# Kernel optimization log

Measured on AMD Instinct MI355X. Metric: run time of the kernel, lower is better.

Reference implementation:

```python
import jax, jax.numpy as jnp
import numpy as np

B, N = 2, 6
FC, FH, FW = 256, 32, 88            # encoder feature shape
ORFH, ORFW = 256, 704               # original image H, W
OUT_C = 128
D_ST, D_END, D_STEP = 1.0, 60.0, 3.0
NXV, NYV, NZV = 256, 256, 1         # BEV voxel grid (x, y, z)
DXV = np.array([0.4, 0.4, 20.0], np.float32)          # dx
BXV = np.array([-51.0, -51.0, 0.0], np.float32)       # bx = bound_lo + dx/2
BN_EPS = 1e-3


def _conv(x, w, b):
    y = jax.lax.conv_general_dilated(x, w, (1, 1), 'SAME',
                                     dimension_numbers=('NCHW', 'OIHW', 'NCHW'))
    return y + b[None, :, None, None]


def _bn(x, scale, bias, mean, var):
    inv = scale / jnp.sqrt(var + BN_EPS)
    return x * inv[None, :, None, None] + (bias - mean * inv)[None, :, None, None]


def _frustum():
    ds = jnp.arange(D_ST, D_END, D_STEP, dtype=jnp.float32)      # (D,)
    xs = jnp.linspace(0.0, ORFW - 1.0, FW)
    ys = jnp.linspace(0.0, ORFH - 1.0, FH)
    f = jnp.stack(jnp.broadcast_arrays(xs[None, None, :], ys[None, :, None],
                                       ds[:, None, None]), axis=-1)  # (D,FH,FW,3)
    return f, ds


def _forward(cam2ego_rot, cam2ego_trans, cam_intrins, post_cam2ego_rot,
             post_cam2ego_trans, img_feats,
             conv1_w, conv1_b, bn1_s, bn1_b, bn1_m, bn1_v,
             conv2_w, conv2_b, bn2_s, bn2_b, bn2_m, bn2_v,
             conv3_w, conv3_b):
    frustum, depth_vals = _frustum()
    D = depth_vals.shape[0]
    # ---- geometry (GaussianLSS.get_geometry) ----
    pts = frustum[None, None] - post_cam2ego_trans[:, :, None, None, None, :]
    inv_post = jnp.linalg.inv(post_cam2ego_rot)                       # (B,N,3,3)
    pts = jnp.einsum('bnij,bndhwj->bndhwi', inv_post, pts)
    pts = jnp.concatenate([pts[..., :2] * pts[..., 2:3], pts[..., 2:3]], -1)
    combine = cam2ego_rot @ jnp.linalg.inv(cam_intrins)
    geometry = (jnp.einsum('bnij,bndhwj->bndhwi', combine, pts)
                + cam2ego_trans[:, :, None, None, None, :])           # (B,N,D,H,W,3)
    # ---- depth net + gaussian depth distribution (get_cam_feature) ----
    x = img_feats.reshape(B * N, FC, FH, FW)
    x = jax.nn.relu(_bn(_conv(x, conv1_w, conv1_b), bn1_s, bn1_b, bn1_m, bn1_v))
    x = jax.nn.relu(_bn(_conv(x, conv2_w, conv2_b), bn2_s, bn2_b, bn2_m, bn2_v))
    x = _conv(x, conv3_w, conv3_b)                                    # (BN, OUT_C+2, H, W)
    mu, log_sigma, feats = x[:, 0], x[:, 1], x[:, 2:]
    sigma = jnp.exp(log_sigma) + 1e-6
    g = jnp.exp(-0.5 * (depth_vals[None, :, None, None] - mu[:, None]) ** 2
                / (sigma[:, None] ** 2))                              # (BN,D,H,W)
    g = g / (jnp.sum(g, axis=1, keepdims=True) + 1e-6)
    vol = g[:, None] * feats[:, :, None]                              # (BN,C,D,H,W)
    vol = vol.reshape(B, N, OUT_C, D, FH, FW).transpose(0, 1, 3, 4, 5, 2)  # (B,N,D,H,W,C)
    # ---- bev_pool: voxelize + scatter-add ----
    dx = jnp.asarray(DXV)
    bx = jnp.asarray(BXV)
    geom = ((geometry - (bx - dx / 2.0)) / dx).astype(jnp.int32)      # trunc like .long()
    gx, gy, gz = geom[..., 0], geom[..., 1], geom[..., 2]
    kept = ((gx >= 0) & (gx < NXV) & (gy >= 0) & (gy < NYV)
            & (gz >= 0) & (gz < NZV))                                 # (B,N,D,H,W)
    bidx = jnp.arange(B, dtype=jnp.int32)[:, None, None, None, None]
    flat = ((bidx * NZV + gz) * NXV + gx) * NYV + gy
    flat = jnp.where(kept, flat, 0)
    w = kept.astype(vol.dtype)
    data = (vol * w[..., None]).reshape(-1, OUT_C)
    bev = jax.ops.segment_sum(data, flat.reshape(-1),
                              num_segments=B * NZV * NXV * NYV)
    # torch: (B,C,Z,X,Y) -> cat(unbind(dim=2), 1) -> (B, Z*C, X, Y)
    bev = bev.reshape(B, NZV, NXV, NYV, OUT_C).transpose(0, 1, 4, 2, 3)
    bev = bev.reshape(B, NZV * OUT_C, NXV, NYV)
    # ---- ref_bev_pool mask ----
    counts = jax.ops.segment_sum(w.reshape(-1), flat.reshape(-1),
                                 num_segments=B * NZV * NXV * NYV)
    mask = jnp.any(counts.reshape(B, NZV, NXV, NYV) > 0, axis=1)      # (B,X,Y) bool
    return bev, mask


def setup_inputs() -> dict:
    key = jax.random.key(0)
    ks = jax.random.split(key, 16)
    # camera->ego rotation: cam z -> ego x, cam x -> -ego y, cam y -> -ego z
    R = jnp.array([[0., 0., 1.], [-1., 0., 0.], [0., -1., 0.]], jnp.float32)
    cam2ego_rot = jnp.tile(R, (B, N, 1, 1)) + 0.01 * jax.random.normal(ks[0], (B, N, 3, 3))
    cam2ego_trans = jax.random.uniform(ks[1], (B, N, 3), minval=-2.0, maxval=2.0)
    K = jnp.array([[500., 0., ORFW / 2.], [0., 500., ORFH / 2.], [0., 0., 1.]], jnp.float32)
    cam_intrins = jnp.tile(K, (B, N, 1, 1))
    post_cam2ego_rot = jnp.tile(jnp.eye(3, dtype=jnp.float32), (B, N, 1, 1)) \
        + 0.005 * jax.random.normal(ks[2], (B, N, 3, 3))
    post_cam2ego_trans = 0.5 * jax.random.normal(ks[3], (B, N, 3))
    img_feats = 0.1 * jax.random.normal(ks[4], (B, N, FC, FH, FW))
    conv3_b = jnp.zeros((OUT_C + 2,)).at[0].set(25.0).at[1].set(2.3)  # mu~25m, sigma~10m
    return dict(
        cam2ego_rot=cam2ego_rot, cam2ego_trans=cam2ego_trans,
        cam_intrins=cam_intrins, post_cam2ego_rot=post_cam2ego_rot,
        post_cam2ego_trans=post_cam2ego_trans, img_feats=img_feats,
        conv1_w=0.02 * jax.random.normal(ks[5], (FC, FC, 3, 3)),
        conv1_b=jnp.zeros((FC,)),
        bn1_s=1.0 + 0.01 * jax.random.normal(ks[6], (FC,)),
        bn1_b=0.01 * jax.random.normal(ks[7], (FC,)),
        bn1_m=0.01 * jax.random.normal(ks[8], (FC,)),
        bn1_v=1.0 + 0.1 * jax.random.uniform(ks[9], (FC,)),
        conv2_w=0.02 * jax.random.normal(ks[10], (FC, FC, 3, 3)),
        conv2_b=jnp.zeros((FC,)),
        bn2_s=1.0 + 0.01 * jax.random.normal(ks[11], (FC,)),
        bn2_b=0.01 * jax.random.normal(ks[12], (FC,)),
        bn2_m=0.01 * jax.random.normal(ks[13], (FC,)),
        bn2_v=1.0 + 0.1 * jax.random.uniform(ks[14], (FC,)),
        conv3_w=0.02 * jax.random.normal(ks[15], (OUT_C + 2, FC, 1, 1)),
        conv3_b=conv3_b,
    )


def reference(cam2ego_rot, cam2ego_trans, cam_intrins, post_cam2ego_rot,
              post_cam2ego_trans, img_feats,
              conv1_w, conv1_b, bn1_s, bn1_b, bn1_m, bn1_v,
              conv2_w, conv2_b, bn2_s, bn2_b, bn2_m, bn2_v,
              conv3_w, conv3_b):
    return _forward(cam2ego_rot, cam2ego_trans, cam_intrins, post_cam2ego_rot,
                    post_cam2ego_trans, img_feats,
                    conv1_w, conv1_b, bn1_s, bn1_b, bn1_m, bn1_v,
                    conv2_w, conv2_b, bn2_s, bn2_b, bn2_m, bn2_v,
                    conv3_w, conv3_b)
```

## Files before the change

### kernel.cpp

```cpp
#include <hip/hip_runtime.h>
#include <math.h>

typedef unsigned short ushort_t;
typedef unsigned int uint_t;

#define NIMG 12
#define NCH  256
#define FH   32
#define FW   88
#define NPIX 2816
#define NDEP 20
#define NOUTC 128
#define NVOX 65536
#define NPTS 675840
#define NKEY 131072
#define BEV_FLOATS 16777216u

#define B_OCC    0u
#define B_A1     4096u
#define B_C1     5120u
#define B_A2     6144u
#define B_C2     7168u
#define B_TOT    278528u
#define B_FEAT   282624u
#define B_RECS   17584128u
#define B_BEV    22990848u
#define B_VCODE  22990848u
#define B_WT     25694208u
#define B_CNT    28397568u
#define B_OFFS   28921856u
#define B_CUR    29446144u
#define B_SPINE  29970432u
#define B_XBF    29972480u
#define B_ACT1   47273984u
#define B_ACT2   64575488u
#define B_WSWZ1  81876992u
#define B_WSWZ2  83056640u
#define B_WSWZ3  84236288u

#define PREP_W2    2304
#define PREP_W3    4608
#define PREP_BN    4752
#define PREP_CAST0 4753
#define PREP_GEOM0 5281
#define PREP_NBLK  7921

typedef __attribute__((ext_vector_type(8))) short bf16x8;
typedef __attribute__((ext_vector_type(4))) float floatx4;
typedef __attribute__((ext_vector_type(4))) uint_t u32x4;

__device__ __forceinline__ ushort_t f2bf(float f) {
    uint_t x = __float_as_uint(f);
    return (ushort_t)((x + 0x7fffu + ((x >> 16) & 1u)) >> 16);
}
__device__ __forceinline__ float bf2f(ushort_t u) {
    return __uint_as_float(((uint_t)u) << 16);
}

__device__ __forceinline__ void inv3x3(const float* __restrict__ M, float* __restrict__ o) {
    float a=M[0],b=M[1],c=M[2],d=M[3],e=M[4],f=M[5],g=M[6],h=M[7],i=M[8];
    float A = e*i - f*h;
    float B = c*h - b*i;
    float C = b*f - c*e;
    float D = f*g - d*i;
    float E = a*i - c*g;
    float F = c*d - a*f;
    float G = d*h - e*g;
    float H = b*g - a*h;
    float I = a*e - b*d;
    float det = a*A + b*D + c*G;
    float id = 1.0f / det;
    o[0]=A*id; o[1]=B*id; o[2]=C*id;
    o[3]=D*id; o[4]=E*id; o[5]=F*id;
    o[6]=G*id; o[7]=H*id; o[8]=I*id;
}

__device__ __forceinline__ void wprep_one(
    const float* __restrict__ w, ushort_t* __restrict__ dst,
    int ntap, int ncib, int ncog, int nco, int nci, int idx, bool split)
{
    int j = idx & 7;
    int l = (idx >> 3) & 63;
    int pairidx = idx >> 9;
    int g = pairidx % ncog;
    int b = (pairidx / ncog) % ncib;
    int t = pairidx / (ncog * ncib);
    int co = g * 16 + (l & 15);
    int ci = b * 32 + (l >> 4) * 8 + j;
    float v = 0.0f;
    if (co < nco) v = w[((size_t)co * nci + ci) * ntap + t];
    ushort_t hi = f2bf(v);
    if (split) {
        dst[(size_t)pairidx * 1024 + l * 8 + j]       = hi;
        dst[(size_t)pairidx * 1024 + 512 + l * 8 + j] = f2bf(v - bf2f(hi));
    } else {
        dst[(size_t)pairidx * 512 + l * 8 + j] = hi;
    }
}

__global__ __launch_bounds__(256) void prep_all_kernel(
    const float* __restrict__ w1, ushort_t* __restrict__ d1,
    const float* __restrict__ w2, ushort_t* __restrict__ d2,
    const float* __restrict__ w3, ushort_t* __restrict__ d3,
    const float* __restrict__ c2e_rot, const float* __restrict__ c2e_trans,
    const float* __restrict__ intrins, const float* __restrict__ post_rot,
    const float* __restrict__ post_trans,
    const float* __restrict__ c1b, const float* __restrict__ s1,
    const float* __restrict__ bb1, const float* __restrict__ m1, const float* __restrict__ v1,
    const float* __restrict__ c2b, const float* __restrict__ s2,
    const float* __restrict__ bb2, const float* __restrict__ m2, const float* __restrict__ v2,
    float* __restrict__ A1, float* __restrict__ C1,
    float* __restrict__ A2, float* __restrict__ C2,
    const float* __restrict__ img_in, ushort_t* __restrict__ xbf_out,
    int* __restrict__ vcode, uint_t* __restrict__ cnt)
{
    __shared__ __align__(16) ushort_t clds[64 * 264];
    int bid = blockIdx.x;
    int t = threadIdx.x;
    if (bid < PREP_W2) {
        wprep_one(w1, d1, 9, 8, 16, 256, 256, bid * 256 + t, false);
    } else if (bid < PREP_W3) {
        wprep_one(w2, d2, 9, 8, 16, 256, 256, (bid - PREP_W2) * 256 + t, false);
    } else if (bid < PREP_BN) {
        int idx = (bid - PREP_W3) * 256 + t;
        if (idx < 36864) wprep_one(w3, d3, 1, 8, 9, 130, 256, idx, true);
    } else if (bid == PREP_BN) {
        float i1 = s1[t] / sqrtf(v1[t] + 1e-3f);
        A1[t] = i1;
        C1[t] = (c1b[t] - m1[t]) * i1 + bb1[t];
        float i2 = s2[t] / sqrtf(v2[t] + 1e-3f);
        A2[t] = i2;
        C2[t] = (c2b[t] - m2[t]) * i2 + bb2[t];
    } else if (bid < PREP_GEOM0) {
        int cblk = bid - PREP_CAST0;
        int img = cblk / 44;
        int px0 = (cblk - img * 44) * 64;
        const float* src = img_in + (size_t)img * NCH * NPIX;
        int pxl = t & 63;
        int cib = t >> 6;
        #pragma unroll 4
        for (int cc = 0; cc < 64; ++cc) {
            int ci = cc * 4 + cib;
            float v = src[(size_t)ci * NPIX + px0 + pxl];
            clds[pxl * 264 + ci] = f2bf(v);
        }
        __syncthreads();
        int wv = t >> 6, lane = t & 63;
        uint2* outv = (uint2*)xbf_out;
        #pragma unroll
        for (int i = 0; i < 16; ++i) {
            int p = wv * 16 + i;
            uint2 val = *(const uint2*)&clds[p * 264 + lane * 4];
            outv[(size_t)(img * NPIX + px0 + p) * 64 + lane] = val;
        }
    } else {
        int i = (bid - PREP_GEOM0) * 256 + t;
        int lane = t & 63;
        int hw  = i % NPIX;
        int tmp = i / NPIX;
        int d   = tmp % NDEP;
        int bn  = tmp / NDEP;
        int h = hw / FW, w = hw - h * FW;
        float ip[9], ki[9], comb[9];
        inv3x3(post_rot + bn * 9, ip);
        inv3x3(intrins  + bn * 9, ki);
        const float* R = c2e_rot + bn * 9;
        #pragma unroll
        for (int r = 0; r < 3; ++r)
            #pragma unroll
            for (int cc = 0; cc < 3; ++cc)
                comb[r*3+cc] = R[r*3+0]*ki[0*3+cc] + R[r*3+1]*ki[1*3+cc] + R[r*3+2]*ki[2*3+cc];
        float xs = (float)w * (703.0f / 87.0f);
        float ys = (float)h * (255.0f / 31.0f);
        float dv = 1.0f + 3.0f * (float)d;
        float fx = xs - post_trans[bn*3+0];
        float fy = ys - post_trans[bn*3+1];
        float fz = dv - post_trans[bn*3+2];
        float p0 = ip[0]*fx + ip[1]*fy + ip[2]*fz;
        float p1 = ip[3]*fx + ip[4]*fy + ip[5]*fz;
        float p2 = ip[6]*fx + ip[7]*fy + ip[8]*fz;
        p0 *= p2; p1 *= p2;
        float gx = comb[0]*p0 + comb[1]*p1 + comb[2]*p2 + c2e_trans[bn*3+0];
        float gy = comb[3]*p0 + comb[4]*p1 + comb[5]*p2 + c2e_trans[bn*3+1];
        float gz = comb[6]*p0 + comb[7]*p1 + comb[8]*p2 + c2e_trans[bn*3+2];
        const float cx = -51.0f - 0.2f, cy = -51.0f - 0.2f, cz = 0.0f - 10.0f;
        int ix = (int)((gx - cx) / 0.4f);
        int iy = (int)((gy - cy) / 0.4f);
        int iz = (int)((gz - cz) / 20.0f);
        bool kept = (ix >= 0) && (ix < 256) && (iy >= 0) && (iy < 256) && (iz == 0);
        int code = kept ? ((ix << 8) | iy) : -1;
        vcode[i] = code;

        int b = bn / 6;
        uint_t key = kept ? (uint_t)((b << 16) | code) : 0xFFFFFFFFu;
        uint_t prevkey = __shfl_up(key, 1);
        bool leader = (lane == 0) || (key != prevkey);
        unsigned long long mask = __ballot(leader);
        if (leader && kept) {
            unsigned long long higher = mask & ~((2ULL << lane) - 1ULL);
            int nxt = higher ? (__ffsll((long long)higher) - 1) : 64;
            atomicAdd(&cnt[key], (uint_t)(nxt - lane));
        }
    }
}

__global__ __launch_bounds__(256, 3) void conv3x3_mfma(
    const ushort_t* __restrict__ in,
    const ushort_t* __restrict__ wswz,
    const float* __restrict__ Abn, const float* __restrict__ Cbn,
    ushort_t* __restrict__ out)
{
    __shared__ __align__(16) ushort_t lds[2][8640];
    int bx = blockIdx.x;
    int cg = blockIdx.y;
    int img = bx >> 5, h = bx & 31;
    int t = threadIdx.x;
    int w = t >> 6, l = t & 63;
    int q = l >> 4, c = l & 15;
    const int n0s[6] = {0, 16, 32, 48, 64, 72};

    for (int i = t; i < 8640; i += 256) ((uint_t*)lds)[i] = 0;

    const u32x4* src4 = (const u32x4*)(in + (size_t)img * NPIX * 256);
    const bf16x8* wsA = (const bf16x8*)wswz;

    int gbase[5], loff[5];
    bool sval[5];
    #pragma unroll
    for (int k = 0; k < 5; ++k) {
        int p = t + k * 256;
        bool valid = (p < 1056);
        int chunk = p >> 2, sub = p & 3;
        int r = chunk / 88;
        int col = chunk - r * 88;
        int hin = h - 1 + r;
        bool inb = valid && (hin >= 0) && (hin < FH);
        sval[k] = inb;
        gbase[k] = inb ? ((hin * 88 + col) * 32 + sub) : 0;
        int cs = col + 1;
        int slot = sub ^ ((cs >> 1) & 3);
        loff[k] = ((r * 90 + cs) * 4 + slot) * 8;
    }

    floatx4 acc[2][6];
    #pragma unroll
    for (int m = 0; m < 2; ++m)
        #pragma unroll
        for (int n = 0; n < 6; ++n)
            acc[m][n] = (floatx4){0.f, 0.f, 0.f, 0.f};

    int g0 = cg * 8 + w * 2;

    __syncthreads();
    #pragma unroll
    for (int k = 0; k < 5; ++k)
        if (sval[k]) *(u32x4*)&lds[0][loff[k]] = src4[gbase[k]];

    int buf = 0;
    for (int kb = 0; kb < 8; ++kb) {
        __syncthreads();
        u32x4 sreg[5];
        if (kb < 7) {
            #pragma unroll
            for (int k = 0; k < 5; ++k)
                if (sval[k]) sreg[k] = src4[gbase[k] + (kb + 1) * 4];
        }
        const bf16x8* B = (const bf16x8*)lds[buf];

        bf16x8 a0, a1;
        {
            int pa = (0 * 8 + kb) * 16;
            a0 = wsA[(size_t)(pa + g0    ) * 64 + l];
            a1 = wsA[(size_t)(pa + g0 + 1) * 64 + l];
        }
        #pragma unroll
        for (int t9 = 0; t9 < 9; ++t9) {
            bf16x8 na0, na1;
            if (t9 < 8) {
                int pa = ((t9 + 1) * 8 + kb) * 16;
                na0 = wsA[(size_t)(pa + g0    ) * 64 + l];
                na1 = wsA[(size_t)(pa + g0 + 1) * 64 + l];
            }
            int ky = t9 / 3, kx = t9 - ky * 3;
            #pragma unroll
            for (int n = 0; n < 6; ++n) {
                int col = n0s[n] + kx + c;
                int slot = q ^ ((col >> 1) & 3);
                bf16x8 b = B[(ky * 90 + col) * 4 + slot];
                acc[0][n] = __builtin_amdgcn_mfma_f32_16x16x32_bf16(a0, b, acc[0][n], 0, 0, 0);
                acc[1][n] = __builtin_amdgcn_mfma_f32_16x16x32_bf16(a1, b, acc[1][n], 0, 0, 0);
            }
            if (t9 < 8) { a0 = na0; a1 = na1; }
        }
        if (kb < 7) {
            #pragma unroll
            for (int k = 0; k < 5; ++k)
                if (sval[k]) *(u32x4*)&lds[buf ^ 1][loff[k]] = sreg[k];
        }
        buf ^= 1;
    }

    #pragma unroll
    for (int m = 0; m < 2; ++m) {
        int cob = cg * 128 + w * 32 + m * 16 + q * 4;
        float ba0 = Abn[cob+0], ba1 = Abn[cob+1], ba2 = Abn[cob+2], ba3 = Abn[cob+3];
        float bc0 = Cbn[cob+0], bc1 = Cbn[cob+1], bc2 = Cbn[cob+2], bc3 = Cbn[cob+3];
        #pragma unroll
        for (int n = 0; n < 6; ++n) {
            if (n == 5 && c < 8) continue;
            int col = n0s[n] + c;
            floatx4 v = acc[m][n];
            uint_t lo = (uint_t)f2bf(fmaxf(v[0]*ba0+bc0, 0.f)) | ((uint_t)f2bf(fmaxf(v[1]*ba1+bc1, 0.f)) << 16);
            uint_t hi = (uint_t)f2bf(fmaxf(v[2]*ba2+bc2, 0.f)) | ((uint_t)f2bf(fmaxf(v[3]*ba3+bc3, 0.f)) << 16);
            uint2 val; val.x = lo; val.y = hi;
            *(uint2*)&out[((size_t)img * NPIX + h * 88 + col) * 256 + cob] = val;
        }
    }
}

__global__ __launch_bounds__(256, 4) void gemm1x1_mfma(
    const ushort_t* __restrict__ act2,
    const ushort_t* __restrict__ wswz3,
    const float* __restrict__ b3,
    ushort_t* __restrict__ feat, float* __restrict__ wt)
{
    int t = threadIdx.x, wv = t >> 6, l = t & 63, q = l >> 4, c = l & 15;
    int n0 = (blockIdx.x * 4 + wv) * 16;
    int px = n0 + c;
    const bf16x8* A = (const bf16x8*)wswz3;
    const bf16x8* B = (const bf16x8*)act2;
    floatx4 acc[9];
    #pragma unroll
    for (int g = 0; g < 9; ++g) acc[g] = (floatx4){0.f, 0.f, 0.f, 0.f};
    for (int kb = 0; kb < 8; ++kb) {
        bf16x8 b = B[(size_t)px * 32 + kb * 4 + q];
        #pragma unroll
        for (int g = 0; g < 9; ++g) {
            size_t pa = (size_t)(kb * 9 + g) * 128;
            acc[g] = __builtin_amdgcn_mfma_f32_16x16x32_bf16(A[pa + l],      b, acc[g], 0, 0, 0);
            acc[g] = __builtin_amdgcn_mfma_f32_16x16x32_bf16(A[pa + 64 + l], b, acc[g], 0, 0, 0);
        }
    }
    #pragma unroll
    for (int g = 0; g < 9; ++g) {
        #pragma unroll
        for (int r = 0; r < 4; ++r) {
            int co = g * 16 + q * 4 + r;
            if (co < 2 || co >= 130) continue;
            feat[(size_t)px * 128 + (co - 2)] = f2bf(acc[g][r] + b3[co]);
        }
    }
    float muv = acc[0][0] + b3[0];
    float lsv = acc[0][1] + b3[1];
    float mu_b  = __shfl(muv, c);
    float sig   = expf(__shfl(lsv, c)) + 1e-6f;
    float ninv2 = -0.5f / (sig * sig);
    float g5[5]; float s = 0.0f;
    #pragma unroll
    for (int j = 0; j < 5; ++j) {
        float dv = 1.0f + 3.0f * (float)(q * 5 + j);
        float df = dv - mu_b;
        g5[j] = expf(df * df * ninv2);
        s += g5[j];
    }
    s += __shfl_xor(s, 16);
    s += __shfl_xor(s, 32);
    float inv = 1.0f / (s + 1e-6f);
    #pragma unroll
    for (int j = 0; j < 5; ++j)
        wt[(size_t)px * NDEP + q * 5 + j] = g5[j] * inv;
}

__global__ __launch_bounds__(256) void scan_block_kernel(
    const uint_t* __restrict__ cnt, uint_t* __restrict__ offs, uint_t* __restrict__ spine)
{
    __shared__ uint_t s[256];
    int t = threadIdx.x;
    int i = blockIdx.x * 256 + t;
    uint_t v = cnt[i];
    s[t] = v;
    __syncthreads();
    #pragma unroll
    for (int off = 1; off < 256; off <<= 1) {
        uint_t add = (t >= off) ? s[t - off] : 0u;
        __syncthreads();
        s[t] += add;
        __syncthreads();
    }
    offs[i] = s[t] - v;
    if (t == 255) spine[blockIdx.x] = s[255];
}

__global__ __launch_bounds__(256) void fixup_kernel(
    uint_t* __restrict__ offs, const uint_t* __restrict__ spine,
    uint_t* __restrict__ cursor, const uint_t* __restrict__ cnt,
    float* __restrict__ mask_out, uint_t* __restrict__ total,
    unsigned char* __restrict__ occ)
{
    __shared__ uint_t red[256];
    int bid = blockIdx.x, t = threadIdx.x;
    uint_t part = 0;
    for (int j = t; j < bid; j += 256) part += spine[j];
    red[t] = part;
    __syncthreads();
    #pragma unroll
    for (int off = 128; off > 0; off >>= 1) {
        if (t < off) red[t] += red[t + off];
        __syncthreads();
    }
    uint_t prefix = red[0];
    int i = bid * 256 + t;
    uint_t o = offs[i] + prefix;
    offs[i] = o;
    cursor[i] = o;
    uint_t n = cnt[i];
    mask_out[i] = (n > 0) ? 1.0f : 0.0f;
    int lane = t & 63, wv = t >> 6;
    unsigned long long any = __ballot(n > 0u);
    if (lane == 0) occ[bid * 4 + wv] = any ? 1 : 0;
    if (i == NKEY - 1) *total = o + n;
}

__global__ __launch_bounds__(256) void scatter_kernel(
    const int* __restrict__ vcode, const float* __restrict__ wt,
    uint_t* __restrict__ cursor, uint2* __restrict__ recs)
{
    int i = blockIdx.x * 256 + threadIdx.x;
    int lane = threadIdx.x & 63;
    int code = vcode[i];
    int hw  = i % NPIX;
    int tmp = i / NPIX;
    int d   = tmp % NDEP;
    int bn  = tmp / NDEP;
    int b   = bn / 6;
    int gp  = bn * NPIX + hw;
    bool active = (code >= 0);
    uint_t key = active ? (uint_t)((b << 16) | code) : 0xFFFFFFFFu;
    uint2 r;
    r.x = ((uint_t)(code & 0xffff) << 16) | (uint_t)gp;
    r.y = active ? __float_as_uint(wt[(size_t)gp * NDEP + d]) : 0u;

    uint_t prevkey = __shfl_up(key, 1);
    bool leader = (lane == 0) || (key != prevkey);
    unsigned long long mask = __ballot(leader);
    uint_t base = 0;
    if (leader && active) {
        unsigned long long higher = mask & ~((2ULL << lane) - 1ULL);
        int nxt = higher ? (__ffsll((long long)higher) - 1) : 64;
        base = atomicAdd(&cursor[key], (uint_t)(nxt - lane));
    }
    unsigned long long lower = mask & ((2ULL << lane) - 1ULL);
    int lead = 63 - __clzll((long long)lower);
    base = __shfl(base, lead);
    if (active) recs[base + (lane - lead)] = r;
}

__global__ __launch_bounds__(256) void segreduce_kernel(
    const uint2* __restrict__ recs, const uint_t* __restrict__ total,
    const uint_t* __restrict__ featu,
    float* __restrict__ bev_tmp)
{
    uint_t R = *total;
    int wid = blockIdx.x * 4 + (threadIdx.x >> 6);
    uint_t start = (uint_t)wid * 64u;
    if (start >= R) return;
    int lane = threadIdx.x & 63;
    uint_t ustart = __builtin_amdgcn_readfirstlane(start);

    uint_t myidx = ustart + (uint_t)lane;
    if (myidx >= R) myidx = R - 1u;
    uint2 mr = recs[myidx];

    uint_t rx0 = (uint_t)__shfl((int)mr.x, 0);
    uint_t gp00 = rx0 & 0xffffu;
    uint_t prevk = ((gp00 >= 16896u) ? 0x10000u : 0u) | (rx0 >> 16);
    float acc0 = 0.f, acc1 = 0.f;

    uint_t fbuf[2][16];
    #pragma unroll
    for (int j = 0; j < 16; ++j) {
        uint_t rx = (uint_t)__shfl((int)mr.x, j);
        fbuf[0][j] = featu[(size_t)(rx & 0xffffu) * 64 + lane];
    }
    #pragma unroll
    for (int b = 0; b < 4; ++b) {
        if (b < 3) {
            #pragma unroll
            for (int j = 0; j < 16; ++j) {
                uint_t rx = (uint_t)__shfl((int)mr.x, (b + 1) * 16 + j);
                fbuf[(b + 1) & 1][j] = featu[(size_t)(rx & 0xffffu) * 64 + lane];
            }
        }
        #pragma unroll
        for (int j = 0; j < 16; ++j) {
            int e = b * 16 + j;
            uint_t rx = (uint_t)__shfl((int)mr.x, e);
            uint_t ry = (uint_t)__shfl((int)mr.y, e);
            uint_t gp = rx & 0xffffu;
            uint_t key = ((gp >= 16896u) ? 0x10000u : 0u) | (rx >> 16);
            float wv = __uint_as_float(ry);
            if (ustart + (uint_t)e >= R) { key = prevk; wv = 0.f; }
            if (key != prevk) {
                float* p = bev_tmp + (size_t)prevk * NOUTC;
                atomicAdd(p + 2 * lane,     acc0);
                atomicAdd(p + 2 * lane + 1, acc1);
                acc0 = acc1 = 0.f;
                prevk = key;
            }
            uint_t fv = fbuf[b & 1][j];
            acc0 = fmaf(wv, bf2f((ushort_t)(fv & 0xffffu)), acc0);
            acc1 = fmaf(wv, bf2f((ushort_t)(fv >> 16)),     acc1);
        }
    }
    float* p = bev_tmp + (size_t)prevk * NOUTC;
    atomicAdd(p + 2 * lane,     acc0);
    atomicAdd(p + 2 * lane + 1, acc1);
}

__global__ __launch_bounds__(256) void transpose_kernel(
    const float* __restrict__ bev_tmp, const unsigned char* __restrict__ occ,
    float* __restrict__ bev_out)
{
    __shared__ float lds[64 * 129];
    int blk = blockIdx.x;
    int b   = blk >> 10;
    int v0  = (blk & 1023) * 64;
    int t   = threadIdx.x;
    float* dst = bev_out + (size_t)b * NOUTC * NVOX + v0;
    if (!occ[blk]) {
        #pragma unroll
        for (int k = 0; k < 32; ++k) {
            int idx = k * 256 + t;
            int vl = idx & 63, ch = idx >> 6;
            dst[(size_t)ch * NVOX + vl] = 0.0f;
        }
        return;
    }
    const float* src = bev_tmp + ((size_t)b * NVOX + v0) * NOUTC;
    #pragma unroll
    for (int k = 0; k < 32; ++k) {
        int idx = k * 256 + t;
        int v = idx >> 7, ch = idx & 127;
        lds[v * 129 + ch] = src[idx];
    }
    __syncthreads();
    #pragma unroll
    for (int k = 0; k < 32; ++k) {
        int idx = k * 256 + t;
        int vl = idx & 63, ch = idx >> 6;
        dst[(size_t)ch * NVOX + vl] = lds[vl * 129 + ch];
    }
}

extern "C" void kernel_launch(void* const* d_in, const int* in_sizes, int n_in,
                              void* d_out, int out_size, void* d_ws, size_t ws_size,
                              hipStream_t stream) {
    const float* c2e_rot    = (const float*)d_in[0];
    const float* c2e_trans  = (const float*)d_in[1];
    const float* intrins    = (const float*)d_in[2];
    const float* post_rot   = (const float*)d_in[3];
    const float* post_trans = (const float*)d_in[4];
    const float* img_feats  = (const float*)d_in[5];
    const float* conv1_w    = (const float*)d_in[6];
    const float* conv1_b    = (const float*)d_in[7];
    const float* bn1_s = (const float*)d_in[8];
    const float* bn1_b = (const float*)d_in[9];
    const float* bn1_m = (const float*)d_in[10];
    const float* bn1_v = (const float*)d_in[11];
    const float* conv2_w = (const float*)d_in[12];
    const float* conv2_b = (const float*)d_in[13];
    const float* bn2_s = (const float*)d_in[14];
    const float* bn2_b = (const float*)d_in[15];
    const float* bn2_m = (const float*)d_in[16];
    const float* bn2_v = (const float*)d_in[17];
    const float* conv3_w = (const float*)d_in[18];
    const float* conv3_b = (const float*)d_in[19];

    char* base = (char*)d_ws;
    unsigned char* occ = (unsigned char*)(base + B_OCC);
    float*    A1     = (float*)(base + B_A1);
    float*    C1     = (float*)(base + B_C1);
    float*    A2     = (float*)(base + B_A2);
    float*    C2     = (float*)(base + B_C2);
    uint_t*   total  = (uint_t*)(base + B_TOT);
    ushort_t* feat   = (ushort_t*)(base + B_FEAT);
    uint2*    recs   = (uint2*)(base + B_RECS);
    float*    bevtmp = (float*)(base + B_BEV);
    int*      vcode  = (int*)(base + B_VCODE);
    float*    wt     = (float*)(base + B_WT);
    uint_t*   cnt    = (uint_t*)(base + B_CNT);
    uint_t*   offs   = (uint_t*)(base + B_OFFS);
    uint_t*   cursor = (uint_t*)(base + B_CUR);
    uint_t*   spine  = (uint_t*)(base + B_SPINE);
    ushort_t* xbf    = (ushort_t*)(base + B_XBF);
    ushort_t* act1   = (ushort_t*)(base + B_ACT1);
    ushort_t* act2   = (ushort_t*)(base + B_ACT2);
    ushort_t* wswz1  = (ushort_t*)(base + B_WSWZ1);
    ushort_t* wswz2  = (ushort_t*)(base + B_WSWZ2);
    ushort_t* wswz3  = (ushort_t*)(base + B_WSWZ3);

    float* bev_out  = (float*)d_out;
    float* mask_out = bev_out + BEV_FLOATS;

    hipMemsetAsync(cnt, 0, NKEY * sizeof(uint_t), stream);
    prep_all_kernel<<<PREP_NBLK, 256, 0, stream>>>(
        conv1_w, wswz1, conv2_w, wswz2, conv3_w, wswz3,
        c2e_rot, c2e_trans, intrins, post_rot, post_trans,
        conv1_b, bn1_s, bn1_b, bn1_m, bn1_v,
        conv2_b, bn2_s, bn2_b, bn2_m, bn2_v,
        A1, C1, A2, C2,
        img_feats, xbf, vcode, cnt);
    conv3x3_mfma<<<dim3(NIMG * 32, 2), 256, 0, stream>>>(xbf,  wswz1, A1, C1, act1);
    conv3x3_mfma<<<dim3(NIMG * 32, 2), 256, 0, stream>>>(act1, wswz2, A2, C2, act2);
    gemm1x1_mfma<<<528, 256, 0, stream>>>(act2, wswz3, conv3_b, feat, wt);
    scan_block_kernel<<<NKEY / 256, 256, 0, stream>>>(cnt, offs, spine);
    fixup_kernel<<<NKEY / 256, 256, 0, stream>>>(offs, spine, cursor, cnt, mask_out, total, occ);
    scatter_kernel<<<NPTS / 256, 256, 0, stream>>>(vcode, wt, cursor, recs);
    hipMemsetAsync(bevtmp, 0, (size_t)BEV_FLOATS * sizeof(float), stream);
    segreduce_kernel<<<(NPTS / 64 + 3) / 4, 256, 0, stream>>>(recs, total, (const uint_t*)feat, bevtmp);
    transpose_kernel<<<2048, 256, 0, stream>>>(bevtmp, occ, bev_out);
}
```

Measured before the change: 351.0 us.

## Accumulate BEV directly in output layout; fuse block scan into 1x1 GEMM launch

The segmented reduction now atomically adds into the channel-major output, which removes the temporary voxel-major BEV buffer, its memset, the occupancy flags and the transpose kernel. The per-block scan of voxel counts runs as extra blocks of the 1x1 GEMM launch, saving one kernel launch. The depth-weight array is stored depth-major so the scatter reads it in a coalesced way. In exchange, the atomics are now strided by NVOX per channel, so each wave's 64 lanes hit scattered addresses instead of one contiguous row.

Result: slower. 506.4 us (+44.3%).

```diff
diff --git a/kernel.cpp b/kernel.cpp
--- a/kernel.cpp
+++ b/kernel.cpp
@@ -14,9 +14,9 @@
 #define NVOX 65536
 #define NPTS 675840
 #define NKEY 131072
+#define NGP  33792
 #define BEV_FLOATS 16777216u
 
-#define B_OCC    0u
 #define B_A1     4096u
 #define B_C1     5120u
 #define B_A2     6144u
@@ -24,7 +24,6 @@
 #define B_TOT    278528u
 #define B_FEAT   282624u
 #define B_RECS   17584128u
-#define B_BEV    22990848u
 #define B_VCODE  22990848u
 #define B_WT     25694208u
 #define B_CNT    28397568u
@@ -44,6 +43,9 @@
 #define PREP_CAST0 4753
 #define PREP_GEOM0 5281
 #define PREP_NBLK  7921
+
+#define GS_SCAN0   528
+#define GS_NBLK    1040
 
 typedef __attribute__((ext_vector_type(8))) short bf16x8;
 typedef __attribute__((ext_vector_type(4))) float floatx4;
@@ -318,13 +320,34 @@
     }
 }
 
-__global__ __launch_bounds__(256, 4) void gemm1x1_mfma(
+__global__ __launch_bounds__(256, 4) void gemm_scan_kernel(
     const ushort_t* __restrict__ act2,
     const ushort_t* __restrict__ wswz3,
     const float* __restrict__ b3,
-    ushort_t* __restrict__ feat, float* __restrict__ wt)
-{
-    int t = threadIdx.x, wv = t >> 6, l = t & 63, q = l >> 4, c = l & 15;
+    ushort_t* __restrict__ feat, float* __restrict__ wt,
+    const uint_t* __restrict__ cnt, uint_t* __restrict__ offs,
+    uint_t* __restrict__ spine)
+{
+    __shared__ uint_t s[256];
+    int t = threadIdx.x;
+    if (blockIdx.x >= GS_SCAN0) {
+        int blk = blockIdx.x - GS_SCAN0;
+        int i = blk * 256 + t;
+        uint_t v = cnt[i];
+        s[t] = v;
+        __syncthreads();
+        #pragma unroll
+        for (int off = 1; off < 256; off <<= 1) {
+            uint_t add = (t >= off) ? s[t - off] : 0u;
+            __syncthreads();
+            s[t] += add;
+            __syncthreads();
+        }
+        offs[i] = s[t] - v;
+        if (t == 255) spine[blk] = s[255];
+        return;
+    }
+    int wv = t >> 6, l = t & 63, q = l >> 4, c = l & 15;
     int n0 = (blockIdx.x * 4 + wv) * 16;
     int px = n0 + c;
     const bf16x8* A = (const bf16x8*)wswz3;
@@ -355,47 +378,26 @@
     float mu_b  = __shfl(muv, c);
     float sig   = expf(__shfl(lsv, c)) + 1e-6f;
     float ninv2 = -0.5f / (sig * sig);
-    float g5[5]; float s = 0.0f;
+    float g5[5]; float sum = 0.0f;
     #pragma unroll
     for (int j = 0; j < 5; ++j) {
         float dv = 1.0f + 3.0f * (float)(q * 5 + j);
         float df = dv - mu_b;
         g5[j] = expf(df * df * ninv2);
-        s += g5[j];
-    }
-    s += __shfl_xor(s, 16);
-    s += __shfl_xor(s, 32);
-    float inv = 1.0f / (s + 1e-6f);
+        sum += g5[j];
+    }
+    sum += __shfl_xor(sum, 16);
+    sum += __shfl_xor(sum, 32);
+    float inv = 1.0f / (sum + 1e-6f);
     #pragma unroll
     for (int j = 0; j < 5; ++j)
-        wt[(size_t)px * NDEP + q * 5 + j] = g5[j] * inv;
-}
-
-__global__ __launch_bounds__(256) void scan_block_kernel(
-    const uint_t* __restrict__ cnt, uint_t* __restrict__ offs, uint_t* __restrict__ spine)
-{
-    __shared__ uint_t s[256];
-    int t = threadIdx.x;
-    int i = blockIdx.x * 256 + t;
-    uint_t v = cnt[i];
-    s[t] = v;
-    __syncthreads();
-    #pragma unroll
-    for (int off = 1; off < 256; off <<= 1) {
-        uint_t add = (t >= off) ? s[t - off] : 0u;
-        __syncthreads();
-        s[t] += add;
-        __syncthreads();
-    }
-    offs[i] = s[t] - v;
-    if (t == 255) spine[blockIdx.x] = s[255];
+        wt[(size_t)(q * 5 + j) * NGP + px] = g5[j] * inv;
 }
 
 __global__ __launch_bounds__(256) void fixup_kernel(
     uint_t* __restrict__ offs, const uint_t* __restrict__ spine,
     uint_t* __restrict__ cursor, const uint_t* __restrict__ cnt,
-    float* __restrict__ mask_out, uint_t* __restrict__ total,
-    unsigned char* __restrict__ occ)
+    float* __restrict__ mask_out, uint_t* __restrict__ total)
 {
     __shared__ uint_t red[256];
     int bid = blockIdx.x, t = threadIdx.x;
@@ -415,9 +417,6 @@
     cursor[i] = o;
     uint_t n = cnt[i];
     mask_out[i] = (n > 0) ? 1.0f : 0.0f;
-    int lane = t & 63, wv = t >> 6;
-    unsigned long long any = __ballot(n > 0u);
-    if (lane == 0) occ[bid * 4 + wv] = any ? 1 : 0;
     if (i == NKEY - 1) *total = o + n;
 }
 
@@ -438,7 +437,7 @@
     uint_t key = active ? (uint_t)((b << 16) | code) : 0xFFFFFFFFu;
     uint2 r;
     r.x = ((uint_t)(code & 0xffff) << 16) | (uint_t)gp;
-    r.y = active ? __float_as_uint(wt[(size_t)gp * NDEP + d]) : 0u;
+    r.y = active ? __float_as_uint(wt[(size_t)d * NGP + gp]) : 0u;
 
     uint_t prevkey = __shfl_up(key, 1);
     bool leader = (lane == 0) || (key != prevkey);
@@ -458,7 +457,7 @@
 __global__ __launch_bounds__(256) void segreduce_kernel(
     const uint2* __restrict__ recs, const uint_t* __restrict__ total,
     const uint_t* __restrict__ featu,
-    float* __restrict__ bev_tmp)
+    float* __restrict__ bev_out)
 {
     uint_t R = *total;
     int wid = blockIdx.x * 4 + (threadIdx.x >> 6);
@@ -501,9 +500,10 @@
             float wv = __uint_as_float(ry);
             if (ustart + (uint_t)e >= R) { key = prevk; wv = 0.f; }
             if (key != prevk) {
-                float* p = bev_tmp + (size_t)prevk * NOUTC;
-                atomicAdd(p + 2 * lane,     acc0);
-                atomicAdd(p + 2 * lane + 1, acc1);
+                float* p = bev_out + (size_t)(prevk >> 16) * (NOUTC * (size_t)NVOX)
+                                   + (prevk & 0xffffu);
+                atomicAdd(p + (size_t)(2 * lane)     * NVOX, acc0);
+                atomicAdd(p + (size_t)(2 * lane + 1) * NVOX, acc1);
                 acc0 = acc1 = 0.f;
                 prevk = key;
             }
@@ -512,44 +512,10 @@
             acc1 = fmaf(wv, bf2f((ushort_t)(fv >> 16)),     acc1);
         }
     }
-    float* p = bev_tmp + (size_t)prevk * NOUTC;
-    atomicAdd(p + 2 * lane,     acc0);
-    atomicAdd(p + 2 * lane + 1, acc1);
-}
-
-__global__ __launch_bounds__(256) void transpose_kernel(
-    const float* __restrict__ bev_tmp, const unsigned char* __restrict__ occ,
-    float* __restrict__ bev_out)
-{
-    __shared__ float lds[64 * 129];
-    int blk = blockIdx.x;
-    int b   = blk >> 10;
-    int v0  = (blk & 1023) * 64;
-    int t   = threadIdx.x;
-    float* dst = bev_out + (size_t)b * NOUTC * NVOX + v0;
-    if (!occ[blk]) {
-        #pragma unroll
-        for (int k = 0; k < 32; ++k) {
-            int idx = k * 256 + t;
-            int vl = idx & 63, ch = idx >> 6;
-            dst[(size_t)ch * NVOX + vl] = 0.0f;
-        }
-        return;
-    }
-    const float* src = bev_tmp + ((size_t)b * NVOX + v0) * NOUTC;
-    #pragma unroll
-    for (int k = 0; k < 32; ++k) {
-        int idx = k * 256 + t;
-        int v = idx >> 7, ch = idx & 127;
-        lds[v * 129 + ch] = src[idx];
-    }
-    __syncthreads();
-    #pragma unroll
-    for (int k = 0; k < 32; ++k) {
-        int idx = k * 256 + t;
-        int vl = idx & 63, ch = idx >> 6;
-        dst[(size_t)ch * NVOX + vl] = lds[vl * 129 + ch];
-    }
+    float* p = bev_out + (size_t)(prevk >> 16) * (NOUTC * (size_t)NVOX)
+                       + (prevk & 0xffffu);
+    atomicAdd(p + (size_t)(2 * lane)     * NVOX, acc0);
+    atomicAdd(p + (size_t)(2 * lane + 1) * NVOX, acc1);
 }
 
 extern "C" void kernel_launch(void* const* d_in, const int* in_sizes, int n_in,
@@ -577,7 +543,6 @@
     const float* conv3_b = (const float*)d_in[19];
 
     char* base = (char*)d_ws;
-    unsigned char* occ = (unsigned char*)(base + B_OCC);
     float*    A1     = (float*)(base + B_A1);
     float*    C1     = (float*)(base + B_C1);
     float*    A2     = (float*)(base + B_A2);
@@ -585,7 +550,6 @@
     uint_t*   total  = (uint_t*)(base + B_TOT);
     ushort_t* feat   = (ushort_t*)(base + B_FEAT);
     uint2*    recs   = (uint2*)(base + B_RECS);
-    float*    bevtmp = (float*)(base + B_BEV);
     int*      vcode  = (int*)(base + B_VCODE);
     float*    wt     = (float*)(base + B_WT);
     uint_t*   cnt    = (uint_t*)(base + B_CNT);
@@ -602,6 +566,7 @@
     float* bev_out  = (float*)d_out;
     float* mask_out = bev_out + BEV_FLOATS;
 
+    hipMemsetAsync(bev_out, 0, (size_t)BEV_FLOATS * sizeof(float), stream);
     hipMemsetAsync(cnt, 0, NKEY * sizeof(uint_t), stream);
     prep_all_kernel<<<PREP_NBLK, 256, 0, stream>>>(
         conv1_w, wswz1, conv2_w, wswz2, conv3_w, wswz3,
@@ -612,11 +577,9 @@
         img_feats, xbf, vcode, cnt);
     conv3x3_mfma<<<dim3(NIMG * 32, 2), 256, 0, stream>>>(xbf,  wswz1, A1, C1, act1);
     conv3x3_mfma<<<dim3(NIMG * 32, 2), 256, 0, stream>>>(act1, wswz2, A2, C2, act2);
-    gemm1x1_mfma<<<528, 256, 0, stream>>>(act2, wswz3, conv3_b, feat, wt);
-    scan_block_kernel<<<NKEY / 256, 256, 0, stream>>>(cnt, offs, spine);
-    fixup_kernel<<<NKEY / 256, 256, 0, stream>>>(offs, spine, cursor, cnt, mask_out, total, occ);
+    gemm_scan_kernel<<<GS_NBLK, 256, 0, stream>>>(act2, wswz3, conv3_b, feat, wt,
+                                                  cnt, offs, spine);
+    fixup_kernel<<<NKEY / 256, 256, 0, stream>>>(offs, spine, cursor, cnt, mask_out, total);
     scatter_kernel<<<NPTS / 256, 256, 0, stream>>>(vcode, wt, cursor, recs);
-    hipMemsetAsync(bevtmp, 0, (size_t)BEV_FLOATS * sizeof(float), stream);
-    segreduce_kernel<<<(NPTS / 64 + 3) / 4, 256, 0, stream>>>(recs, total, (const uint_t*)feat, bevtmp);
-    transpose_kernel<<<2048, 256, 0, stream>>>(bevtmp, occ, bev_out);
-}
+    segreduce_kernel<<<(NPTS / 64 + 3) / 4, 256, 0, stream>>>(recs, total, (const uint_t*)feat, bev_out);
+}
```
